# Performance work log

Hardware: AMD Instinct MI355X
Metric: run time of the kernel (lower is better)

## Reference

```python
import jax, jax.numpy as jnp
import numpy as np

B, S, H, O, K = 32, 2048, 768, 768, 64


def setup_inputs() -> dict:
    key = jax.random.key(0)
    k0, k1, k2, k3, k4 = jax.random.split(key, 5)
    hidden = jax.random.normal(k0, (B, S, H), dtype=jnp.float32)
    token_idxs = jnp.sort(jax.random.randint(k1, (B, K), 0, S), axis=1)
    subject_hidden = jax.random.normal(k2, (B, H), dtype=jnp.float32)
    Wa = jax.random.normal(k3, (2 * H, 1), dtype=jnp.float32) * 0.02
    ba = jnp.zeros((1,), dtype=jnp.float32)
    Wo = jax.random.normal(k4, (H, O), dtype=jnp.float32) * 0.02
    bo = jnp.zeros((O,), dtype=jnp.float32)
    return {"hidden": hidden, "token_idxs": token_idxs, "subject_hidden": subject_hidden,
            "Wa": Wa, "ba": ba, "Wo": Wo, "bo": bo}


def reference(hidden, token_idxs, subject_hidden, Wa, ba, Wo, bo):
    b, s, h = hidden.shape
    # binary token mask [B,S] from per-example index lists (duplicates collapse to 1)
    mask = jnp.zeros((b, s), hidden.dtype).at[jnp.arange(b)[:, None], token_idxs].set(1.0)
    m3 = mask[:, :, None]                                  # [B,S,1]
    masked = hidden * m3                                   # masked_hidden
    subj_rep = subject_hidden[:, None, :] * m3             # broadcast + mask, no repeat
    # alignment_model(concat(subj, masked)) done as split matmul to avoid [B,S,2H]
    scores = subj_rep @ Wa[:h] + masked @ Wa[h:] + ba      # [B,S,1]
    # masked softmax over the selected tokens only (dim=0 over selected entries == seq axis)
    logits = jnp.where(m3 > 0, scores, jnp.float32(-1e9))
    attention_weights = jax.nn.softmax(logits, axis=1) * m3  # exact zeros off-mask
    pooled = jnp.einsum("bsh,bs->bh", masked, attention_weights[:, :, 0])
    transformed = jnp.tanh(pooled @ Wo + bo)
    return transformed, attention_weights
```

## Files before the change

### kernel.cpp

```cpp
#include <hip/hip_runtime.h>
#include <cmath>

#define Bb 32
#define Ss 2048
#define Hh 768
#define Oo 768
#define Kk 64

__global__ __launch_bounds__(256) void scores_kernel(
    const float* __restrict__ hidden,
    const int*   __restrict__ idxs,
    const float* __restrict__ Wa,
    float* __restrict__ scores,
    float* __restrict__ aw_out)
{
    const int tid  = threadIdx.x;
    const int lane = tid & 63;
    const int wid  = blockIdx.x * 4 + (tid >> 6);
    const int gid  = blockIdx.x * 256 + tid;

    if (gid < (Bb * Ss / 4))
        ((float4*)aw_out)[gid] = make_float4(0.f, 0.f, 0.f, 0.f);

    const int b = wid >> 6;
    const int j = wid & 63;
    const int t_idx = idxs[b * Kk + j];

    const float4* row4 = (const float4*)(hidden + ((size_t)b * Ss + t_idx) * Hh);
    const float4* wa4  = (const float4*)(Wa + Hh);
    float p = 0.f;
    #pragma unroll
    for (int t = 0; t < 3; ++t) {
        const float4 r = row4[lane + 64 * t];
        const float4 w = wa4[lane + 64 * t];
        p += r.x * w.x + r.y * w.y + r.z * w.z + r.w * w.w;
    }
    #pragma unroll
    for (int m = 32; m >= 1; m >>= 1) p += __shfl_xor(p, m);
    if (lane == 0) scores[wid] = p;
}

__global__ __launch_bounds__(64) void softmax_kernel(
    const int*   __restrict__ idxs,
    const float* __restrict__ subj,
    const float* __restrict__ Wa,
    const float* __restrict__ ba,
    const float* __restrict__ scores,
    float* __restrict__ aw,
    float* __restrict__ aw_out)
{
    const int b = blockIdx.x;
    const int j = threadIdx.x;

    const float4* s4  = (const float4*)(subj + b * Hh);
    const float4* wa4 = (const float4*)Wa;
    float p = 0.f;
    #pragma unroll
    for (int t = 0; t < 3; ++t) {
        const float4 r = s4[j + 64 * t];
        const float4 w = wa4[j + 64 * t];
        p += r.x * w.x + r.y * w.y + r.z * w.z + r.w * w.w;
    }
    #pragma unroll
    for (int m = 32; m >= 1; m >>= 1) p += __shfl_xor(p, m);
    const float sconst = p + ba[0];

    const int  myidx   = idxs[b * Kk + j];
    const int  previdx = (j > 0) ? idxs[b * Kk + j - 1] : -1;
    const bool active  = (j == 0) || (myidx != previdx);

    float sc = active ? (scores[b * Kk + j] + sconst) : -3.0e38f;
    float mx = sc;
    #pragma unroll
    for (int m = 32; m >= 1; m >>= 1) mx = fmaxf(mx, __shfl_xor(mx, m));
    const float e = active ? expf(sc - mx) : 0.f;
    float sum = e;
    #pragma unroll
    for (int m = 32; m >= 1; m >>= 1) sum += __shfl_xor(sum, m);
    const float w = e / sum;

    aw[b * Kk + j] = w;
    if (active) aw_out[(size_t)b * Ss + myidx] = w;
}

__global__ __launch_bounds__(1024) void pool_gemm_kernel(
    const float* __restrict__ hidden,
    const int*   __restrict__ idxs,
    const float* __restrict__ aw,
    const float* __restrict__ Wo,
    const float* __restrict__ bo,
    float* __restrict__ out)
{
    const int b   = blockIdx.x / 3;
    const int oc  = blockIdx.x % 3;
    const int tid = threadIdx.x;

    __shared__ float s_aw[Kk];
    __shared__ int   s_idx[Kk];
    __shared__ float s_pool[Hh];
    __shared__ float s_part[4 * 256];

    if (tid < Kk) {
        s_aw[tid]  = aw[b * Kk + tid];
        s_idx[tid] = idxs[b * Kk + tid];
    }
    __syncthreads();

    if (tid < Hh) {
        float acc = 0.f;
        #pragma unroll 8
        for (int j = 0; j < Kk; ++j)
            acc += s_aw[j] * hidden[((size_t)b * Ss + s_idx[j]) * Hh + tid];
        s_pool[tid] = acc;
    }
    __syncthreads();

    const int ol = tid & 255;
    const int o  = oc * 256 + ol;
    const int hg = tid >> 8;
    const int h0 = hg * 192;
    float acc = 0.f;
    #pragma unroll 8
    for (int h = h0; h < h0 + 192; ++h)
        acc = fmaf(s_pool[h], Wo[h * Oo + o], acc);
    s_part[hg * 256 + ol] = acc;
    __syncthreads();

    if (tid < 256) {
        const int oo = oc * 256 + tid;
        const float s = s_part[tid] + s_part[256 + tid] + s_part[512 + tid]
                      + s_part[768 + tid] + bo[oo];
        out[b * Oo + oo] = tanhf(s);
    }
}

extern "C" void kernel_launch(void* const* d_in, const int* in_sizes, int n_in,
                              void* d_out, int out_size, void* d_ws, size_t ws_size,
                              hipStream_t stream) {
    const float* hidden = (const float*)d_in[0];
    const int*   idxs   = (const int*)d_in[1];
    const float* subj   = (const float*)d_in[2];
    const float* Wa     = (const float*)d_in[3];
    const float* ba     = (const float*)d_in[4];
    const float* Wo     = (const float*)d_in[5];
    const float* bo     = (const float*)d_in[6];

    float* out    = (float*)d_out;
    float* aw_out = out + Bb * Oo;
    float* scores = (float*)d_ws;
    float* aw     = scores + Bb * Kk;

    scores_kernel <<<512, 256, 0, stream>>>(hidden, idxs, Wa, scores, aw_out);
    softmax_kernel<<<Bb, 64, 0, stream>>>(idxs, subj, Wa, ba, scores, aw, aw_out);
    pool_gemm_kernel<<<Bb * 3, 1024, 0, stream>>>(hidden, idxs, aw, Wo, bo, out);
}
```

Measured before the change: 261.8 us.

## Fuse scores, softmax and pooling per batch; split GEMM across more blocks

Merges the score, softmax and pooling stages into one kernel with one 256-thread block per batch element, with intermediates kept in shared memory. This removes one launch and the global round trips for scores and weights. The output GEMM now runs as its own kernel with 6 column tiles per batch instead of 3, which raises the block count. In exchange, the fused stage runs on only 32 blocks, so less of the GPU works in parallel on the gathers.

```diff
diff --git a/kernel.cpp b/kernel.cpp
--- a/kernel.cpp
+++ b/kernel.cpp
@@ -7,130 +7,135 @@
 #define Oo 768
 #define Kk 64
 
-__global__ __launch_bounds__(256) void scores_kernel(
+__global__ __launch_bounds__(256) void attn_pool_kernel(
     const float* __restrict__ hidden,
-    const int*   __restrict__ idxs,
-    const float* __restrict__ Wa,
-    float* __restrict__ scores,
-    float* __restrict__ aw_out)
-{
-    const int tid  = threadIdx.x;
-    const int lane = tid & 63;
-    const int wid  = blockIdx.x * 4 + (tid >> 6);
-    const int gid  = blockIdx.x * 256 + tid;
-
-    if (gid < (Bb * Ss / 4))
-        ((float4*)aw_out)[gid] = make_float4(0.f, 0.f, 0.f, 0.f);
-
-    const int b = wid >> 6;
-    const int j = wid & 63;
-    const int t_idx = idxs[b * Kk + j];
-
-    const float4* row4 = (const float4*)(hidden + ((size_t)b * Ss + t_idx) * Hh);
-    const float4* wa4  = (const float4*)(Wa + Hh);
-    float p = 0.f;
-    #pragma unroll
-    for (int t = 0; t < 3; ++t) {
-        const float4 r = row4[lane + 64 * t];
-        const float4 w = wa4[lane + 64 * t];
-        p += r.x * w.x + r.y * w.y + r.z * w.z + r.w * w.w;
-    }
-    #pragma unroll
-    for (int m = 32; m >= 1; m >>= 1) p += __shfl_xor(p, m);
-    if (lane == 0) scores[wid] = p;
-}
-
-__global__ __launch_bounds__(64) void softmax_kernel(
     const int*   __restrict__ idxs,
     const float* __restrict__ subj,
     const float* __restrict__ Wa,
     const float* __restrict__ ba,
-    const float* __restrict__ scores,
-    float* __restrict__ aw,
+    float* __restrict__ pooled,
     float* __restrict__ aw_out)
 {
-    const int b = blockIdx.x;
-    const int j = threadIdx.x;
+    const int b    = blockIdx.x;
+    const int tid  = threadIdx.x;
+    const int lane = tid & 63;
+    const int w    = tid >> 6;
 
-    const float4* s4  = (const float4*)(subj + b * Hh);
-    const float4* wa4 = (const float4*)Wa;
-    float p = 0.f;
-    #pragma unroll
-    for (int t = 0; t < 3; ++t) {
-        const float4 r = s4[j + 64 * t];
-        const float4 w = wa4[j + 64 * t];
-        p += r.x * w.x + r.y * w.y + r.z * w.z + r.w * w.w;
+    __shared__ float s_sc[Kk];
+    __shared__ float s_aw[Kk];
+    __shared__ int   s_idx[Kk];
+    __shared__ float s_sconst;
+
+    if (tid < Kk) s_idx[tid] = idxs[b * Kk + tid];
+
+    float4* z4 = (float4*)(aw_out + (size_t)b * Ss);
+    z4[tid]       = make_float4(0.f, 0.f, 0.f, 0.f);
+    z4[tid + 256] = make_float4(0.f, 0.f, 0.f, 0.f);
+
+    if (w == 0) {
+        const float4* s4  = (const float4*)(subj + b * Hh);
+        const float4* wa4 = (const float4*)Wa;
+        float p = 0.f;
+        #pragma unroll
+        for (int t = 0; t < 3; ++t) {
+            const float4 r = s4[lane + 64 * t];
+            const float4 q = wa4[lane + 64 * t];
+            p += r.x * q.x + r.y * q.y + r.z * q.z + r.w * q.w;
+        }
+        #pragma unroll
+        for (int m = 32; m >= 1; m >>= 1) p += __shfl_xor(p, m);
+        if (lane == 0) s_sconst = p + ba[0];
     }
-    #pragma unroll
-    for (int m = 32; m >= 1; m >>= 1) p += __shfl_xor(p, m);
-    const float sconst = p + ba[0];
+    __syncthreads();
 
-    const int  myidx   = idxs[b * Kk + j];
-    const int  previdx = (j > 0) ? idxs[b * Kk + j - 1] : -1;
-    const bool active  = (j == 0) || (myidx != previdx);
+    {
+        const float4* wa4 = (const float4*)(Wa + Hh);
+        const float4 q0 = wa4[lane];
+        const float4 q1 = wa4[lane + 64];
+        const float4 q2 = wa4[lane + 128];
+        #pragma unroll 2
+        for (int jj = 0; jj < 16; ++jj) {
+            const int j = w * 16 + jj;
+            const float4* r4 =
+                (const float4*)(hidden + ((size_t)b * Ss + s_idx[j]) * Hh);
+            const float4 r0 = r4[lane];
+            const float4 r1 = r4[lane + 64];
+            const float4 r2 = r4[lane + 128];
+            float p = r0.x * q0.x + r0.y * q0.y + r0.z * q0.z + r0.w * q0.w
+                    + r1.x * q1.x + r1.y * q1.y + r1.z * q1.z + r1.w * q1.w
+                    + r2.x * q2.x + r2.y * q2.y + r2.z * q2.z + r2.w * q2.w;
+            #pragma unroll
+            for (int m = 32; m >= 1; m >>= 1) p += __shfl_xor(p, m);
+            if (lane == 0) s_sc[j] = p;
+        }
+    }
+    __syncthreads();
 
-    float sc = active ? (scores[b * Kk + j] + sconst) : -3.0e38f;
-    float mx = sc;
-    #pragma unroll
-    for (int m = 32; m >= 1; m >>= 1) mx = fmaxf(mx, __shfl_xor(mx, m));
-    const float e = active ? expf(sc - mx) : 0.f;
-    float sum = e;
-    #pragma unroll
-    for (int m = 32; m >= 1; m >>= 1) sum += __shfl_xor(sum, m);
-    const float w = e / sum;
+    if (tid < Kk) {
+        const float sc = s_sc[tid] + s_sconst;
+        const bool active = (tid == 0) || (s_idx[tid] != s_idx[tid - 1]);
+        float v = active ? sc : -3.0e38f;
+        float mx = v;
+        #pragma unroll
+        for (int m = 32; m >= 1; m >>= 1) mx = fmaxf(mx, __shfl_xor(mx, m));
+        const float e = active ? expf(sc - mx) : 0.f;
+        float sum = e;
+        #pragma unroll
+        for (int m = 32; m >= 1; m >>= 1) sum += __shfl_xor(sum, m);
+        const float wgt = e / sum;
+        s_aw[tid] = wgt;
+        if (active) aw_out[(size_t)b * Ss + s_idx[tid]] = wgt;
+    }
+    __syncthreads();
 
-    aw[b * Kk + j] = w;
-    if (active) aw_out[(size_t)b * Ss + myidx] = w;
+    {
+        float a0 = 0.f, a1 = 0.f, a2 = 0.f;
+        #pragma unroll 8
+        for (int j = 0; j < Kk; ++j) {
+            const float wj = s_aw[j];
+            const float* row = hidden + ((size_t)b * Ss + s_idx[j]) * Hh;
+            a0 = fmaf(wj, row[tid],       a0);
+            a1 = fmaf(wj, row[tid + 256], a1);
+            a2 = fmaf(wj, row[tid + 512], a2);
+        }
+        pooled[b * Hh + tid]       = a0;
+        pooled[b * Hh + tid + 256] = a1;
+        pooled[b * Hh + tid + 512] = a2;
+    }
 }
 
-__global__ __launch_bounds__(1024) void pool_gemm_kernel(
-    const float* __restrict__ hidden,
-    const int*   __restrict__ idxs,
-    const float* __restrict__ aw,
+__global__ __launch_bounds__(1024) void gemm_kernel(
+    const float* __restrict__ pooled,
     const float* __restrict__ Wo,
     const float* __restrict__ bo,
     float* __restrict__ out)
 {
-    const int b   = blockIdx.x / 3;
-    const int oc  = blockIdx.x % 3;
+    const int b   = blockIdx.x / 6;
+    const int oc  = blockIdx.x % 6;
     const int tid = threadIdx.x;
 
-    __shared__ float s_aw[Kk];
-    __shared__ int   s_idx[Kk];
     __shared__ float s_pool[Hh];
-    __shared__ float s_part[4 * 256];
+    __shared__ float s_part[8 * 128];
 
-    if (tid < Kk) {
-        s_aw[tid]  = aw[b * Kk + tid];
-        s_idx[tid] = idxs[b * Kk + tid];
-    }
+    if (tid < Hh) s_pool[tid] = pooled[b * Hh + tid];
     __syncthreads();
 
-    if (tid < Hh) {
-        float acc = 0.f;
-        #pragma unroll 8
-        for (int j = 0; j < Kk; ++j)
-            acc += s_aw[j] * hidden[((size_t)b * Ss + s_idx[j]) * Hh + tid];
-        s_pool[tid] = acc;
-    }
+    const int ol = tid & 127;
+    const int o  = oc * 128 + ol;
+    const int hg = tid >> 7;
+    const int h0 = hg * 96;
+    float acc = 0.f;
+    #pragma unroll 8
+    for (int h = h0; h < h0 + 96; ++h)
+        acc = fmaf(s_pool[h], Wo[h * Oo + o], acc);
+    s_part[hg * 128 + ol] = acc;
     __syncthreads();
 
-    const int ol = tid & 255;
-    const int o  = oc * 256 + ol;
-    const int hg = tid >> 8;
-    const int h0 = hg * 192;
-    float acc = 0.f;
-    #pragma unroll 8
-    for (int h = h0; h < h0 + 192; ++h)
-        acc = fmaf(s_pool[h], Wo[h * Oo + o], acc);
-    s_part[hg * 256 + ol] = acc;
-    __syncthreads();
-
-    if (tid < 256) {
-        const int oo = oc * 256 + tid;
-        const float s = s_part[tid] + s_part[256 + tid] + s_part[512 + tid]
-                      + s_part[768 + tid] + bo[oo];
-        out[b * Oo + oo] = tanhf(s);
+    if (tid < 128) {
+        float s = bo[oc * 128 + tid];
+        #pragma unroll
+        for (int g = 0; g < 8; ++g) s += s_part[g * 128 + tid];
+        out[b * Oo + oc * 128 + tid] = tanhf(s);
     }
 }
 
@@ -147,10 +152,8 @@
 
     float* out    = (float*)d_out;
     float* aw_out = out + Bb * Oo;
-    float* scores = (float*)d_ws;
-    float* aw     = scores + Bb * Kk;
+    float* pooled = (float*)d_ws;
 
-    scores_kernel <<<512, 256, 0, stream>>>(hidden, idxs, Wa, scores, aw_out);
-    softmax_kernel<<<Bb, 64, 0, stream>>>(idxs, subj, Wa, ba, scores, aw, aw_out);
-    pool_gemm_kernel<<<Bb * 3, 1024, 0, stream>>>(hidden, idxs, aw, Wo, bo, out);
+    attn_pool_kernel<<<Bb, 256, 0, stream>>>(hidden, idxs, subj, Wa, ba, pooled, aw_out);
+    gemm_kernel<<<Bb * 6, 1024, 0, stream>>>(pooled, Wo, bo, out);
 }
```

After: 261.9 us. No clear change (+0.1%).
